# Optimization experiments

Hardware: AMD Instinct MI355X
Metric: run time of the kernel (lower is better)

## Reference

```python
import jax, jax.numpy as jnp
import numpy as np

B, N, D = 4, 4096, 1024
H, HD = 16, 64            # num_heads, head_dim (dim // num_heads)
K_ANCHOR = 256
SCALE = 1.0 / np.sqrt(float(HD))


def setup_inputs() -> dict:
    key = jax.random.key(0)
    ks = jax.random.split(key, 12)
    init = lambda k, shape, fan_in: jax.random.normal(k, shape, jnp.float32) * (1.0 / np.sqrt(fan_in))
    return {
        "x": jax.random.normal(ks[0], (B, N, D), jnp.float32),
        "Wq": init(ks[1], (D, H * HD), D), "bq": jnp.zeros((H * HD,), jnp.float32),
        "Wk": init(ks[2], (D, H * HD), D), "bk": jnp.zeros((H * HD,), jnp.float32),
        "Wv": init(ks[3], (D, H * HD), D), "bv": jnp.zeros((H * HD,), jnp.float32),
        "Wqt": init(ks[4], (D, D), D),     "bqt": jnp.zeros((D,), jnp.float32),
        "Wo": init(ks[5], (H * HD, D), H * HD), "bo": jnp.zeros((D,), jnp.float32),
        "num_anchor_tokens": K_ANCHOR,
    }


def _split_heads(t):
    # [B, S, H*HD] -> [B, H, S, HD]
    b, s, _ = t.shape
    return t.reshape(b, s, H, HD).transpose(0, 2, 1, 3)


def reference(x, Wq, bq, Wk, bk, Wv, bv, Wqt, bqt, Wo, bo, num_anchor_tokens):
    K = num_anchor_tokens  # static python int
    anchors = x[:, :K]     # [B, K, D]
    queries = x[:, K:]     # [B, N-K, D]

    q_a = anchors @ Wq + bq           # [B, K, H*HD]
    k_a = anchors @ Wk + bk           # [B, K, H*HD]
    v_a = anchors @ Wv + bv           # [B, K, H*HD]
    q_q = queries @ Wqt + bqt         # [B, N-K, H*HD] (dim == H*HD)

    q = _split_heads(jnp.concatenate([q_a, q_q], axis=1))  # [B, H, N, HD]
    k = _split_heads(k_a)                                  # [B, H, K, HD]
    v = _split_heads(v_a)                                  # [B, H, K, HD]

    scores = jnp.einsum("bhnd,bhkd->bhnk", q, k) * SCALE   # [B, H, N, K]
    weights = jax.nn.softmax(scores, axis=-1)
    ctx = jnp.einsum("bhnk,bhkd->bhnd", weights, v)        # [B, H, N, HD]
    ctx = ctx.transpose(0, 2, 1, 3).reshape(x.shape[0], x.shape[1], H * HD)
    return ctx @ Wo + bo               # [B, N, D]
```

## Files before the change

kernel.cpp:

```cpp
#include <hip/hip_runtime.h>
#include <stdint.h>
#include <stddef.h>


typedef _Float16 v8hf __attribute__((ext_vector_type(8)));
typedef _Float16 h4   __attribute__((ext_vector_type(4)));
typedef float    f32x4 __attribute__((ext_vector_type(4)));

#define ATT_SCALE 0.125f
#define LOG2E     1.44269504088896340736f

__device__ __forceinline__ void async16(const void* g, void* l) {
  __builtin_amdgcn_global_load_lds(
      (const __attribute__((address_space(1))) void*)g,
      (__attribute__((address_space(3))) void*)l,
      16, 0, 0);
}

__global__ __launch_bounds__(256) void cvt_kernel(const float* __restrict__ src,
                                                  _Float16* __restrict__ dst, int n) {
  int i = (blockIdx.x * 256 + threadIdx.x) * 4;
  if (i + 3 < n) {
    float4 v = *(const float4*)(src + i);
    h4 o; o[0] = (_Float16)v.x; o[1] = (_Float16)v.y; o[2] = (_Float16)v.z; o[3] = (_Float16)v.w;
    *(h4*)(dst + i) = o;
  }
}

struct TPArgs { const float* src[5]; _Float16* dst[5]; };

__global__ __launch_bounds__(256) void transpose5_k(TPArgs a) {
  __shared__ _Float16 t[32][33];
  const int z = blockIdx.z;
  const float* __restrict__ src = a.src[z];
  _Float16* __restrict__ dst = a.dst[z];
  const int bx = blockIdx.x * 32, by = blockIdx.y * 32;
  const int x = threadIdx.x;
  for (int yy = threadIdx.y; yy < 32; yy += 8)
    t[yy][x] = (_Float16)src[(size_t)(by + yy) * 1024 + bx + x];
  __syncthreads();
  for (int yy = threadIdx.y; yy < 32; yy += 8)
    dst[(size_t)(bx + yy) * 1024 + by + x] = t[x][yy];
}

template <typename OutT>
__global__ __launch_bounds__(256) void gemm64(
    const _Float16* __restrict__ A, const _Float16* __restrict__ Bt,
    const float* __restrict__ bias0, const float* __restrict__ bias1,
    const float* __restrict__ bias2,
    OutT* __restrict__ out0, _Float16* __restrict__ out1, _Float16* __restrict__ out2,
    int rowsPerBatch, int rowStart, int mode)
{
  __shared__ __attribute__((aligned(16))) _Float16 As[64 * 32];
  __shared__ __attribute__((aligned(16))) _Float16 Bs[128 * 32];

  const int tid  = threadIdx.x;
  const int wave = tid >> 6, lane = tid & 63;
  const int quad = lane >> 4, l16 = lane & 15;
  const int wr = wave >> 1, wc = wave & 1;

  const int gx = gridDim.x;
  const int lin = blockIdx.y * gx + blockIdx.x;
  const int x8 = lin & 7, j = lin >> 3;
  const int bx = j % gx;
  const int by = x8 * (gridDim.y >> 3) + j / gx;

  const int srow = lane >> 2;
  const int skol = (((lane & 3) ^ ((lane >> 3) & 3)) * 8);

  auto gRowOf = [&](int m) -> int {
    int b = m / rowsPerBatch;
    int r = m - b * rowsPerBatch;
    return b * 4096 + rowStart + r;
  };

  const int bc0 = wave * 2, bc1 = bc0 + 1;
  const _Float16* aS  = A  + (size_t)gRowOf(by * 64 + wave * 16 + srow) * 1024 + skol;
  const _Float16* bS0 = Bt + (size_t)(bx * 128 + bc0 * 16 + srow) * 1024 + skol;
  const _Float16* bS1 = Bt + (size_t)(bx * 128 + bc1 * 16 + srow) * 1024 + skol;
  _Float16* aD  = As + wave * 512;
  _Float16* bD0 = Bs + bc0 * 512;
  _Float16* bD1 = Bs + bc1 * 512;

  const int fblk = (quad ^ ((l16 >> 1) & 3)) * 8;

  f32x4 acc[2][4];
  #pragma unroll
  for (int i = 0; i < 2; i++)
    #pragma unroll
    for (int jj = 0; jj < 4; jj++)
      acc[i][jj] = f32x4{0.f, 0.f, 0.f, 0.f};

  for (int k0 = 0; k0 < 1024; k0 += 32) {
    __syncthreads();
    async16(aS  + k0, aD);
    async16(bS0 + k0, bD0);
    async16(bS1 + k0, bD1);
    __syncthreads();

    v8hf af[2], bfr[4];
    #pragma unroll
    for (int mt = 0; mt < 2; mt++)
      af[mt] = *(const v8hf*)(As + (wr * 32 + mt * 16 + l16) * 32 + fblk);
    #pragma unroll
    for (int nt = 0; nt < 4; nt++)
      bfr[nt] = *(const v8hf*)(Bs + (wc * 64 + nt * 16 + l16) * 32 + fblk);
    #pragma unroll
    for (int mt = 0; mt < 2; mt++)
      #pragma unroll
      for (int nt = 0; nt < 4; nt++)
        acc[mt][nt] = __builtin_amdgcn_mfma_f32_16x16x32_f16(af[mt], bfr[nt], acc[mt][nt], 0, 0, 0);
  }

  const int colBase = bx * 128 + wc * 64;
  const int rowBase = by * 64 + wr * 32;
  #pragma unroll
  for (int mt = 0; mt < 2; mt++) {
    #pragma unroll
    for (int r = 0; r < 4; r++) {
      int m = rowBase + mt * 16 + quad * 4 + r;
      int b = m / rowsPerBatch;
      int rr = m - b * rowsPerBatch;
      #pragma unroll
      for (int nt = 0; nt < 4; nt++) {
        int col = colBase + nt * 16 + l16;
        float v = acc[mt][nt][r];
        if (mode == 0) {
          v += bias0[col];
          out0[(size_t)(b * 4096 + rowStart + rr) * 1024 + col] = (OutT)v;
        } else {
          if (col < 1024) {
            v += bias0[col];
            out0[(size_t)(b * 4096 + rr) * 1024 + col] = (OutT)v;
          } else if (col < 2048) {
            int c2 = col - 1024;
            v += bias1[c2];
            out1[(size_t)(b * 256 + rr) * 1024 + c2] = (_Float16)v;
          } else {
            int c2 = col - 2048;
            v += bias2[c2];
            out2[(size_t)((b * 16 + (c2 >> 6)) * 64 + (c2 & 63)) * 256 + rr] = (_Float16)v;
          }
        }
      }
    }
  }
}

__global__ __launch_bounds__(256) void attn_kernel(
    const _Float16* __restrict__ q, const _Float16* __restrict__ k,
    const _Float16* __restrict__ vt, _Float16* __restrict__ ctx)
{
  __shared__ __attribute__((aligned(16))) _Float16 KP[256 * 64];
  __shared__ __attribute__((aligned(16))) _Float16 Vs[64 * 256];

  const int tid  = threadIdx.x;
  const int wave = tid >> 6, lane = tid & 63;
  const int quad = lane >> 4, l16 = lane & 15;
  const int bid = blockIdx.x;
  const int qt = bid & 63, h = (bid >> 6) & 15, b = bid >> 10;

  const int fq = (l16 ^ (l16 >> 1)) & 7;

  const _Float16* kbase = k + (size_t)b * 256 * 1024 + h * 64;
  {
    const int s = lane >> 3;
    const int p = lane & 7;
    #pragma unroll
    for (int i = 0; i < 8; i++) {
      int c = wave * 8 + i;
      int row = c * 8 + s;
      int f = (row ^ (row >> 1)) & 7;
      int dblk = p ^ f;
      async16(kbase + (size_t)row * 1024 + dblk * 8, KP + c * 512);
    }
  }

  const int qrow = qt * 64 + wave * 16 + l16;
  const _Float16* qbase = q + (size_t)(b * 4096 + qrow) * 1024 + h * 64 + quad * 8;
  v8hf a0 = *(const v8hf*)(qbase);
  v8hf a1 = *(const v8hf*)(qbase + 32);

  f32x4 s[16];
  #pragma unroll
  for (int t = 0; t < 16; t++) s[t] = f32x4{0.f, 0.f, 0.f, 0.f};

  __syncthreads();

  #pragma unroll
  for (int t = 0; t < 16; t++) {
    const _Float16* rbase = KP + (t * 16 + l16) * 64;
    int pb0 = (quad ^ fq) * 8;
    v8hf b0 = *(const v8hf*)(rbase + pb0);
    v8hf b1 = *(const v8hf*)(rbase + (pb0 ^ 32));
    s[t] = __builtin_amdgcn_mfma_f32_16x16x32_f16(a0, b0, s[t], 0, 0, 0);
    s[t] = __builtin_amdgcn_mfma_f32_16x16x32_f16(a1, b1, s[t], 0, 0, 0);
  }

  const float ce = ATT_SCALE * LOG2E;
  float inv[4];
  #pragma unroll
  for (int r = 0; r < 4; r++) {
    float m = s[0][r];
    #pragma unroll
    for (int t = 1; t < 16; t++) m = fmaxf(m, s[t][r]);
    m = fmaxf(m, __shfl_xor(m, 1));
    m = fmaxf(m, __shfl_xor(m, 2));
    m = fmaxf(m, __shfl_xor(m, 4));
    m = fmaxf(m, __shfl_xor(m, 8));
    float sum = 0.f;
    #pragma unroll
    for (int t = 0; t < 16; t++) {
      float e = exp2f((s[t][r] - m) * ce);
      s[t][r] = e;
      sum += e;
    }
    sum += __shfl_xor(sum, 1);
    sum += __shfl_xor(sum, 2);
    sum += __shfl_xor(sum, 4);
    sum += __shfl_xor(sum, 8);
    inv[r] = 1.0f / sum;
  }

  __syncthreads();

  const _Float16* vbase = vt + (size_t)(b * 16 + h) * 16384;
  {
    const int p = lane & 31;
    #pragma unroll
    for (int i = 0; i < 8; i++) {
      int c = wave * 8 + i;
      int d = c * 2 + (lane >> 5);
      int f = (d ^ (d >> 1)) & 7;
      int kblk = p ^ f;
      async16(vbase + d * 256 + kblk * 8, Vs + c * 512);
    }
  }

  #pragma unroll
  for (int r = 0; r < 4; r++) {
    int qr = wave * 16 + quad * 4 + r;
    int fp = (qr ^ (qr >> 1)) & 7;
    _Float16* prow = KP + qr * 256;
    #pragma unroll
    for (int t = 0; t < 16; t++) {
      int key = t * 16 + l16;
      prow[(((key >> 3) ^ fp) * 8) + (key & 7)] = (_Float16)(s[t][r] * inv[r]);
    }
  }

  __syncthreads();

  f32x4 o[4];
  #pragma unroll
  for (int nt = 0; nt < 4; nt++) o[nt] = f32x4{0.f, 0.f, 0.f, 0.f};
  #pragma unroll
  for (int c = 0; c < 8; c++) {
    int kblk = c * 4 + quad;
    v8hf pa = *(const v8hf*)(KP + (wave * 16 + l16) * 256 + (kblk ^ fq) * 8);
    #pragma unroll
    for (int nt = 0; nt < 4; nt++) {
      v8hf vb = *(const v8hf*)(Vs + (nt * 16 + l16) * 256 + (kblk ^ fq) * 8);
      o[nt] = __builtin_amdgcn_mfma_f32_16x16x32_f16(pa, vb, o[nt], 0, 0, 0);
    }
  }

  _Float16* obase = ctx + (size_t)(b * 4096 + qt * 64 + wave * 16 + quad * 4) * 1024 + h * 64;
  #pragma unroll
  for (int nt = 0; nt < 4; nt++)
    #pragma unroll
    for (int r = 0; r < 4; r++)
      obase[(size_t)r * 1024 + nt * 16 + l16] = (_Float16)o[nt][r];
}

extern "C" void kernel_launch(void* const* d_in, const int* in_sizes, int n_in,
                              void* d_out, int out_size, void* d_ws, size_t ws_size,
                              hipStream_t stream)
{
  (void)in_sizes; (void)n_in; (void)out_size; (void)ws_size;

  const float* x   = (const float*)d_in[0];
  const float* Wq  = (const float*)d_in[1];
  const float* bq  = (const float*)d_in[2];
  const float* Wk  = (const float*)d_in[3];
  const float* bk  = (const float*)d_in[4];
  const float* Wv  = (const float*)d_in[5];
  const float* bv  = (const float*)d_in[6];
  const float* Wqt = (const float*)d_in[7];
  const float* bqt = (const float*)d_in[8];
  const float* Wo  = (const float*)d_in[9];
  const float* bo  = (const float*)d_in[10];

  char* ws = (char*)d_ws;
  _Float16* xh    = (_Float16*)(ws);
  _Float16* WtQKV = (_Float16*)(ws + (32ll << 20));
  _Float16* WtQT  = (_Float16*)(ws + (38ll << 20));
  _Float16* WtO   = (_Float16*)(ws + (40ll << 20));
  _Float16* qbuf  = (_Float16*)(ws + (42ll << 20));
  _Float16* kbuf  = (_Float16*)(ws + (74ll << 20));
  _Float16* vtb   = (_Float16*)(ws + (76ll << 20));
  _Float16* ctxb  = (_Float16*)(ws + (78ll << 20));
  float* outp = (float*)d_out;

  const int nx = 4 * 4096 * 1024;
  cvt_kernel<<<nx / 1024, 256, 0, stream>>>(x, xh, nx);

  TPArgs tpa;
  tpa.src[0] = Wq;  tpa.dst[0] = WtQKV;
  tpa.src[1] = Wk;  tpa.dst[1] = WtQKV + 1024 * 1024;
  tpa.src[2] = Wv;  tpa.dst[2] = WtQKV + 2 * 1024 * 1024;
  tpa.src[3] = Wqt; tpa.dst[3] = WtQT;
  tpa.src[4] = Wo;  tpa.dst[4] = WtO;
  transpose5_k<<<dim3(32, 32, 5), dim3(32, 8), 0, stream>>>(tpa);

  gemm64<_Float16><<<dim3(24, 16), 256, 0, stream>>>(xh, WtQKV, bq, bk, bv,
                                                     qbuf, kbuf, vtb, 256, 0, 1);
  gemm64<_Float16><<<dim3(8, 240), 256, 0, stream>>>(xh, WtQT, bqt, nullptr, nullptr,
                                                     qbuf, nullptr, nullptr, 3840, 256, 0);
  attn_kernel<<<4096, 256, 0, stream>>>(qbuf, kbuf, vtb, ctxb);
  gemm64<float><<<dim3(8, 256), 256, 0, stream>>>(ctxb, WtO, bo, nullptr, nullptr,
                                                  outp, nullptr, nullptr, 4096, 0, 0);
}
```

Before: 358.6 us.

## Add 256x256-tile GEMM with 4-stage async LDS pipeline for large projections

Adds a new gemm256 kernel that uses 256x256 output tiles, 512 threads, a 4-deep ring of async global-to-LDS loads with XOR-swizzled layout, and a workgroup-id swizzle for L2 locality. The kernel replaces the 64-tile GEMM for the query-transform projection and the output projection. Larger tiles raise arithmetic intensity and cut redundant global loads, and the deeper prefetch hides latency. In exchange it holds 128 accumulator registers per thread and uses large LDS, which lowers occupancy. The grids are also small (240 and 256 workgroups), which may leave some CUs underused.

```diff
diff --git a/kernel.cpp b/kernel.cpp
--- a/kernel.cpp
+++ b/kernel.cpp
@@ -41,6 +41,109 @@
   __syncthreads();
   for (int yy = threadIdx.y; yy < 32; yy += 8)
     dst[(size_t)(bx + yy) * 1024 + by + x] = t[x][yy];
+}
+
+template <typename OutT>
+__global__ __launch_bounds__(512, 2) void gemm256(
+    const _Float16* __restrict__ A, const _Float16* __restrict__ Bt,
+    const float* __restrict__ bias, OutT* __restrict__ out,
+    int rowsPerBatch, int rowStart)
+{
+  __shared__ __attribute__((aligned(16))) _Float16 As[4 * 256 * 32];
+  __shared__ __attribute__((aligned(16))) _Float16 Bs[4 * 256 * 32];
+
+  const int tid  = threadIdx.x;
+  const int wave = tid >> 6, lane = tid & 63;
+  const int quad = lane >> 4, l16 = lane & 15;
+  const int wr = wave >> 2, wc = wave & 3;
+
+  const int nwg = gridDim.x * gridDim.y;
+  const int lin = blockIdx.y * 4 + blockIdx.x;
+  const int swz = (lin & 7) * (nwg >> 3) + (lin >> 3);
+  const int bx = swz & 3, by = swz >> 2;
+
+  const int lrow = lane >> 2, lblk = lane & 3;
+
+  auto gRowOf = [&](int m) -> int {
+    int b = m / rowsPerBatch;
+    return b * 4096 + rowStart + (m - b * rowsPerBatch);
+  };
+
+  const int tr0 = wave * 16 + lrow;
+  const int tr1 = 128 + tr0;
+  const _Float16* aS0 = A  + (size_t)gRowOf(by * 256 + tr0) * 1024 + (lblk ^ ((tr0 >> 1) & 3)) * 8;
+  const _Float16* aS1 = A  + (size_t)gRowOf(by * 256 + tr1) * 1024 + (lblk ^ ((tr1 >> 1) & 3)) * 8;
+  const _Float16* bS0 = Bt + (size_t)(bx * 256 + tr0) * 1024 + (lblk ^ ((tr0 >> 1) & 3)) * 8;
+  const _Float16* bS1 = Bt + (size_t)(bx * 256 + tr1) * 1024 + (lblk ^ ((tr1 >> 1) & 3)) * 8;
+
+  auto stage = [&](int t) {
+    const int k0 = t * 32;
+    _Float16* ad = As + (t & 3) * 8192 + wave * 512;
+    _Float16* bd = Bs + (t & 3) * 8192 + wave * 512;
+    async16(aS0 + k0, ad);
+    async16(aS1 + k0, ad + 4096);
+    async16(bS0 + k0, bd);
+    async16(bS1 + k0, bd + 4096);
+  };
+
+  const int fblk = (quad ^ ((l16 >> 1) & 3)) * 8;
+
+  f32x4 acc[8][4];
+  #pragma unroll
+  for (int i = 0; i < 8; i++)
+    #pragma unroll
+    for (int j = 0; j < 4; j++)
+      acc[i][j] = f32x4{0.f, 0.f, 0.f, 0.f};
+
+  stage(0); stage(1); stage(2);
+
+  #pragma unroll 1
+  for (int t = 0; t < 32; ++t) {
+    if (t < 30)       asm volatile("s_waitcnt vmcnt(8)" ::: "memory");
+    else if (t == 30) asm volatile("s_waitcnt vmcnt(4)" ::: "memory");
+    else              asm volatile("s_waitcnt vmcnt(0)" ::: "memory");
+    __builtin_amdgcn_s_barrier();
+    __builtin_amdgcn_sched_barrier(0);
+    asm volatile("" ::: "memory");
+
+    if (t + 3 < 32) stage(t + 3);
+
+    const _Float16* Ab = As + (t & 3) * 8192;
+    const _Float16* Bb = Bs + (t & 3) * 8192;
+    v8hf af[8], bf[4];
+    #pragma unroll
+    for (int nt = 0; nt < 4; nt++)
+      bf[nt] = *(const v8hf*)(Bb + (wc * 64 + nt * 16 + l16) * 32 + fblk);
+    #pragma unroll
+    for (int mt = 0; mt < 8; mt++)
+      af[mt] = *(const v8hf*)(Ab + (wr * 128 + mt * 16 + l16) * 32 + fblk);
+
+    __builtin_amdgcn_s_setprio(1);
+    #pragma unroll
+    for (int mt = 0; mt < 8; mt++)
+      #pragma unroll
+      for (int nt = 0; nt < 4; nt++)
+        acc[mt][nt] = __builtin_amdgcn_mfma_f32_16x16x32_f16(af[mt], bf[nt], acc[mt][nt], 0, 0, 0);
+    __builtin_amdgcn_s_setprio(0);
+  }
+
+  const int colBase = bx * 256 + wc * 64;
+  const int rowBase = by * 256 + wr * 128;
+  #pragma unroll
+  for (int mt = 0; mt < 8; mt++) {
+    #pragma unroll
+    for (int r = 0; r < 4; r++) {
+      int m = rowBase + mt * 16 + quad * 4 + r;
+      int b = m / rowsPerBatch;
+      int rr = m - b * rowsPerBatch;
+      #pragma unroll
+      for (int nt = 0; nt < 4; nt++) {
+        int col = colBase + nt * 16 + l16;
+        float v = acc[mt][nt][r] + bias[col];
+        out[(size_t)(b * 4096 + rowStart + rr) * 1024 + col] = (OutT)v;
+      }
+    }
+  }
 }
 
 template <typename OutT>
@@ -315,9 +418,9 @@
 
   gemm64<_Float16><<<dim3(24, 16), 256, 0, stream>>>(xh, WtQKV, bq, bk, bv,
                                                      qbuf, kbuf, vtb, 256, 0, 1);
-  gemm64<_Float16><<<dim3(8, 240), 256, 0, stream>>>(xh, WtQT, bqt, nullptr, nullptr,
-                                                     qbuf, nullptr, nullptr, 3840, 256, 0);
+  gemm256<_Float16><<<dim3(4, 60), 512, 0, stream>>>(xh, WtQT, bqt,
+                                                     qbuf, 3840, 256);
   attn_kernel<<<4096, 256, 0, stream>>>(qbuf, kbuf, vtb, ctxb);
-  gemm64<float><<<dim3(8, 256), 256, 0, stream>>>(ctxb, WtO, bo, nullptr, nullptr,
-                                                  outp, nullptr, nullptr, 4096, 0, 0);
-}
+  gemm256<float><<<dim3(4, 64), 512, 0, stream>>>(ctxb, WtO, bo,
+                                                  outp, 4096, 0);
+}
```

Result: faster. 331.5 us (-7.6%).
